# Kernel optimization log

Measured on AMD Instinct MI355X. Metric: run time of the kernel, lower is better.

## Reference

```python
import jax, jax.numpy as jnp
import numpy as np

UNITS = 512
N_CLASSES = 10
N_FEAT = 3
R_ON = 0.05      # open ratio of the phased-LSTM time gate
ALPHA = 0.001    # leak rate when gate is closed


def setup_inputs() -> dict:
    key = jax.random.key(0)
    ks = jax.random.split(key, 16)
    B, T, F, U, C = 512, 1024, N_FEAT, UNITS, N_CLASSES
    inputs = jax.random.normal(ks[0], (B, T, F), dtype=jnp.float32)
    # irregular, monotonically increasing observation times
    gaps = jax.random.uniform(ks[1], (B, T), dtype=jnp.float32, minval=0.01, maxval=1.0)
    times = jnp.cumsum(gaps, axis=1)
    sc_in = 1.0 / np.sqrt(F)
    sc_u = 1.0 / np.sqrt(U)
    params = {
        'W0': jax.random.normal(ks[2], (F, 4 * U), jnp.float32) * sc_in,
        'U0': jax.random.normal(ks[3], (U, 4 * U), jnp.float32) * sc_u,
        'b0': jnp.zeros((4 * U,), jnp.float32),
        'tau0': jnp.exp(jax.random.uniform(ks[4], (U,), jnp.float32, np.log(10.0), np.log(1000.0))),
        's0': jax.random.uniform(ks[5], (U,), jnp.float32, 0.0, 100.0),
        'W1': jax.random.normal(ks[6], (U, 4 * U), jnp.float32) * sc_u,
        'U1': jax.random.normal(ks[7], (U, 4 * U), jnp.float32) * sc_u,
        'b1': jnp.zeros((4 * U,), jnp.float32),
        'tau1': jnp.exp(jax.random.uniform(ks[8], (U,), jnp.float32, np.log(10.0), np.log(1000.0))),
        's1': jax.random.uniform(ks[9], (U,), jnp.float32, 0.0, 100.0),
        'Wfc': jax.random.normal(ks[10], (U, C), jnp.float32) * sc_u,
        'bfc': jnp.zeros((C,), jnp.float32),
    }
    return dict(inputs=inputs, times=times, **params)


def _plstm_cell(x, t, h, c, W, U, b, tau, s):
    # x:[B,in], t:[B], h,c:[B,U]; standard LSTM gates + phased time gate
    z = x @ W + h @ U + b                     # [B,4U]
    i, f, g, o = jnp.split(z, 4, axis=-1)
    i = jax.nn.sigmoid(i)
    f = jax.nn.sigmoid(f)
    g = jnp.tanh(g)
    o = jax.nn.sigmoid(o)
    c_cand = f * c + i * g
    h_cand = o * jnp.tanh(c_cand)
    # time gate: phase of each unit's oscillation at time t
    phi = jnp.mod(t[:, None] - s, tau) / tau  # [B,U] in [0,1)
    k = jnp.where(phi < 0.5 * R_ON, 2.0 * phi / R_ON,
        jnp.where(phi < R_ON, 2.0 - 2.0 * phi / R_ON, ALPHA * phi))
    c_new = k * c_cand + (1.0 - k) * c
    h_new = k * h_cand + (1.0 - k) * h
    return h_new, c_new


def reference(inputs, times, W0, U0, b0, tau0, s0, W1, U1, b1, tau1, s1, Wfc, bfc):
    B = inputs.shape[0]
    Uh = W0.shape[1] // 4
    h0 = jnp.zeros((B, Uh), inputs.dtype)
    init = (h0, h0, h0, h0)  # (h0, c0, h1, c1)

    def step(carry, xt):
        h_0, c_0, h_1, c_1 = carry
        x, t = xt
        h_0, c_0 = _plstm_cell(x, t, h_0, c_0, W0, U0, b0, tau0, s0)
        h_1, c_1 = _plstm_cell(h_0, t, h_1, c_1, W1, U1, b1, tau1, s1)
        y = jax.nn.softmax(h_1 @ Wfc + bfc, axis=-1)
        return (h_0, c_0, h_1, c_1), y

    xs = (jnp.swapaxes(inputs, 0, 1), jnp.swapaxes(times, 0, 1))  # time-major
    _, preds = jax.lax.scan(step, init, xs)   # [T,B,C]
    return jnp.transpose(preds, (1, 0, 2))     # [B,T,C]
```

## Files before the change

kernel.cpp:

```cpp
#include <hip/hip_runtime.h>
#include <hip/hip_bf16.h>
#include <math.h>

#define TDIM 1024
#define UDIM 512
#define NG   2048
#define NBLK 208

typedef __attribute__((ext_vector_type(8))) short short8;
typedef __attribute__((ext_vector_type(4))) float float4v;

#define OFF_U0T   ((size_t)0)
#define SZ_U0T    ((size_t)NG*UDIM*2)
#define OFF_W1U1T (OFF_U0T + SZ_U0T)
#define SZ_W1U1T  ((size_t)NG*1024*2)
#define OFF_W0P   (OFF_W1U1T + SZ_W1U1T)
#define SZ_W0P    ((size_t)3*NG*4)
#define OFF_B0P   (OFF_W0P + SZ_W0P)
#define OFF_B1P   (OFF_B0P + (size_t)NG*4)
#define OFF_STATE (OFF_B1P + (size_t)NG*4)
#define SZ_HB     ((size_t)512*UDIM*2)
#define SZ_HF     ((size_t)512*UDIM*4)
#define OFF_H0B   (OFF_STATE)
#define OFF_H1B   (OFF_H0B + 4*SZ_HB)
#define OFF_H1F   (OFF_H1B + 4*SZ_HB)
#define OFF_CNT   (OFF_H1F + 4*SZ_HF)
#define STATE_BYTES (8*SZ_HB + 4*SZ_HF + 4096)

#define HSLOT ((size_t)512*UDIM)
#define FSLOT ((size_t)512*UDIM)

__device__ __forceinline__ float sigm(float x) { return 1.0f / (1.0f + expf(-x)); }

__device__ __forceinline__ void gload16(const void* g, void* l) {
    __builtin_amdgcn_global_load_lds(
        (const __attribute__((address_space(1))) void*)g,
        (__attribute__((address_space(3))) void*)l, 16, 0, 17);
}

__device__ __forceinline__ void store_u16_llc(void* p, unsigned short v) {
    asm volatile("global_store_short %0, %1, off sc0 sc1" :: "v"(p), "v"(v) : "memory");
}
__device__ __forceinline__ void store_f32_llc(void* p, float v) {
    asm volatile("global_store_dword %0, %1, off sc0 sc1" :: "v"(p), "v"(v) : "memory");
}

__device__ __forceinline__ void wait_ge(unsigned* p, int tgt, unsigned& seen) {
    if ((int)seen >= tgt) return;
    unsigned v = __hip_atomic_load(p, __ATOMIC_RELAXED, __HIP_MEMORY_SCOPE_AGENT);
    while ((int)v < tgt) {
        __builtin_amdgcn_s_sleep(1);
        v = __hip_atomic_load(p, __ATOMIC_RELAXED, __HIP_MEMORY_SCOPE_AGENT);
    }
    seen = v;
}

__device__ __forceinline__ void signal(unsigned* p) {
    asm volatile("s_waitcnt vmcnt(0)" ::: "memory");
    __hip_atomic_fetch_add(p, 1u, __ATOMIC_RELAXED, __HIP_MEMORY_SCOPE_AGENT);
}

__device__ __forceinline__ void cell_update(float zi, float zf, float zg, float zo,
                                            float tt, float tv, float sv,
                                            float& cp, float& hp)
{
    float ig = sigm(zi), fg = sigm(zf), gg = tanhf(zg), og = sigm(zo);
    float cc = fg * cp + ig * gg;
    float hc = og * tanhf(cc);
    float ph = fmodf(tt - sv, tv);
    ph = (ph < 0.0f ? ph + tv : ph) / tv;
    float kg = (ph < 0.025f) ? (ph * 40.0f)
             : (ph < 0.05f ? 2.0f - ph * 40.0f : 0.001f * ph);
    cp = kg * cc + (1.0f - kg) * cp;
    hp = kg * hc + (1.0f - kg) * hp;
}

__global__ void prep_kernel(const float* __restrict__ W0, const float* __restrict__ U0,
                            const float* __restrict__ b0, const float* __restrict__ W1,
                            const float* __restrict__ U1, const float* __restrict__ b1,
                            char* __restrict__ ws)
{
    int idx = blockIdx.x * 256 + threadIdx.x;
    int n = idx >> 10;
    int k = idx & 1023;
    int oc = (n & 3) * UDIM + (n >> 2);
    __hip_bfloat16* U0t = (__hip_bfloat16*)(ws + OFF_U0T);
    __hip_bfloat16* Wc  = (__hip_bfloat16*)(ws + OFF_W1U1T);
    float* W0p = (float*)(ws + OFF_W0P);
    float* b0p = (float*)(ws + OFF_B0P);
    float* b1p = (float*)(ws + OFF_B1P);
    if (k < 512) U0t[(size_t)n * 512 + k] = __float2bfloat16(U0[(size_t)k * NG + oc]);
    float wv = (k < 512) ? W1[(size_t)k * NG + oc] : U1[(size_t)(k - 512) * NG + oc];
    Wc[(size_t)n * 1024 + k] = __float2bfloat16(wv);
    if (k < 3) W0p[k * NG + n] = W0[(size_t)k * NG + oc];
    if (k == 0) { b0p[n] = b0[oc]; b1p[n] = b1[oc]; }
}

__device__ void layer0_persist(char* smem, int blk,
    const float* __restrict__ inputs, const float* __restrict__ times,
    const float* __restrict__ tau0, const float* __restrict__ s0v, char* __restrict__ ws)
{
    const int msl = blk >> 4, nsl = blk & 15;
    unsigned* cnt = (unsigned*)(ws + OFF_CNT);
    unsigned* P0 = cnt + msl * 32;
    unsigned* P1 = cnt + 128 + msl * 32;
    unsigned seen0 = 0, seen1 = 0;
    const int tid = threadIdx.x;
    const int wave = tid >> 6, lane = tid & 63, lr = lane & 15, lq = lane >> 4;
    const int mg = wave >> 2, nw = wave & 3;
    const int colbase = nsl * 128 + nw * 32;

    const __hip_bfloat16* U0t = (const __hip_bfloat16*)(ws + OFF_U0T);
    const float* b0p = (const float*)(ws + OFF_B0P);
    const float* W0p = (const float*)(ws + OFF_W0P);
    __hip_bfloat16* h0b = (__hip_bfloat16*)(ws + OFF_H0B);

    short8 Bf[32];
#pragma unroll
    for (int nf = 0; nf < 2; ++nf)
#pragma unroll
        for (int kk = 0; kk < 16; ++kk)
            Bf[nf * 16 + kk] = *(const short8*)(U0t +
                (size_t)(colbase + nf * 16 + lr) * 512 + kk * 32 + lq * 8);

    const int cu = tid & 31, crb = tid >> 5;
    const int uu = nsl * 32 + cu;
    const int pcc = nsl * 128 + cu * 4;
    const float4v bias4 = *(const float4v*)(b0p + pcc);
    const float4v w0x = *(const float4v*)(W0p + pcc);
    const float4v w0y = *(const float4v*)(W0p + NG + pcc);
    const float4v w0z = *(const float4v*)(W0p + 2 * NG + pcc);
    const float tv = tau0[uu], sv = s0v[uu];

    float c0r[8], h0r[8];
#pragma unroll
    for (int i = 0; i < 8; ++i) { c0r[i] = 0.0f; h0r[i] = 0.0f; }

    const int g_row = tid >> 2;
    const int g_q   = (tid & 3) ^ ((g_row >> 1) & 3);

    for (int s = 0; s < TDIM; ++s) {
        if (tid == 0) {
            wait_ge(P0, 16 * s, seen0);
            if (s >= 4) wait_ge(P1, 32 * (s - 3), seen1);
        }
        __syncthreads();

        const __hip_bfloat16* Arow = h0b + ((size_t)((s + 3) & 3)) * HSLOT +
            (size_t)(msl * 128 + g_row) * 512 + g_q * 8;
        __hip_bfloat16* h0w = h0b + ((size_t)(s & 3)) * HSLOT;
#pragma unroll
        for (int j = 0; j < 7; ++j)
            gload16(Arow + j * 32, smem + j * 8192 + wave * 1024);

        const float4v z4 = {0.0f, 0.0f, 0.0f, 0.0f};
        float4v acc[4][2];
#pragma unroll
        for (int mf = 0; mf < 4; ++mf) { acc[mf][0] = z4; acc[mf][1] = z4; }

#pragma unroll
        for (int j = 0; j < 16; ++j) {
            asm volatile("s_waitcnt vmcnt(%0)" :: "i"((j + 7 < 16) ? 6 : (15 - j)) : "memory");
            __builtin_amdgcn_s_barrier();
            __builtin_amdgcn_sched_barrier(0);
            if (j + 7 < 16)
                gload16(Arow + (j + 7) * 32, smem + ((j + 7) & 7) * 8192 + wave * 1024);
            const short* sA = (const short*)(smem + (j & 7) * 8192);
            short8 aF[4];
#pragma unroll
            for (int mf = 0; mf < 4; ++mf) {
                int row = mg * 64 + mf * 16 + lr;
                int q = lq ^ ((row >> 1) & 3);
                aF[mf] = *(const short8*)(sA + row * 32 + q * 8);
            }
#pragma unroll
            for (int mf = 0; mf < 4; ++mf) {
                acc[mf][0] = __builtin_amdgcn_mfma_f32_16x16x32_bf16(aF[mf], Bf[j],      acc[mf][0], 0, 0, 0);
                acc[mf][1] = __builtin_amdgcn_mfma_f32_16x16x32_bf16(aF[mf], Bf[16 + j], acc[mf][1], 0, 0, 0);
            }
        }
        __syncthreads();
        float* Z = (float*)smem;
#pragma unroll
        for (int pass = 0; pass < 2; ++pass) {
            if (mg == pass) {
#pragma unroll
                for (int mf = 0; mf < 4; ++mf)
#pragma unroll
                    for (int nf = 0; nf < 2; ++nf)
#pragma unroll
                        for (int i = 0; i < 4; ++i)
                            Z[(mf * 16 + lq * 4 + i) * 132 + nw * 32 + nf * 16 + lr] = acc[mf][nf][i];
            }
            __syncthreads();
#pragma unroll
            for (int cc = 0; cc < 4; ++cc) {
                int rl = crb + 16 * cc;
                int b = msl * 128 + pass * 64 + rl;
                float4v z = *(const float4v*)(Z + rl * 132 + cu * 4);
                const float* xp = inputs + ((size_t)b * TDIM + s) * 3;
                float x0 = xp[0], x1 = xp[1], x2 = xp[2];
                float zi = z[0] + bias4[0] + x0 * w0x[0] + x1 * w0y[0] + x2 * w0z[0];
                float zf = z[1] + bias4[1] + x0 * w0x[1] + x1 * w0y[1] + x2 * w0z[1];
                float zg = z[2] + bias4[2] + x0 * w0x[2] + x1 * w0y[2] + x2 * w0z[2];
                float zo = z[3] + bias4[3] + x0 * w0x[3] + x1 * w0y[3] + x2 * w0z[3];
                float tt = times[(size_t)b * TDIM + s];
                cell_update(zi, zf, zg, zo, tt, tv, sv, c0r[pass * 4 + cc], h0r[pass * 4 + cc]);
                __hip_bfloat16 hb = __float2bfloat16(h0r[pass * 4 + cc]);
                store_u16_llc(h0w + (size_t)b * 512 + uu, *(unsigned short*)&hb);
            }
            __syncthreads();
        }
        if (tid == 0) signal(P0);
    }
}

__device__ void layer1_persist(char* smem, int blk,
    const float* __restrict__ times,
    const float* __restrict__ tau1, const float* __restrict__ s1v, char* __restrict__ ws)
{
    const int m8 = blk >> 4, nsl = blk & 15;
    const int grp = m8 >> 1;
    unsigned* cnt = (unsigned*)(ws + OFF_CNT);
    unsigned* P0 = cnt + grp * 32;
    unsigned* P1 = cnt + 128 + grp * 32;
    unsigned* PF = cnt + 256 + grp * 32;
    unsigned seen0 = 0, seen1 = 0, seenF = 0;
    const int tid = threadIdx.x;
    const int wave = tid >> 6, lane = tid & 63, lr = lane & 15, lq = lane >> 4;
    const int kg = wave >> 2, nw = wave & 3;
    const int colbase = nsl * 128 + nw * 32;

    const __hip_bfloat16* Wc = (const __hip_bfloat16*)(ws + OFF_W1U1T);
    const float* b1p = (const float*)(ws + OFF_B1P);
    __hip_bfloat16* h0b = (__hip_bfloat16*)(ws + OFF_H0B);
    __hip_bfloat16* h1b = (__hip_bfloat16*)(ws + OFF_H1B);
    float* h1f = (float*)(ws + OFF_H1F);

    short8 Bf[32];
#pragma unroll
    for (int nf = 0; nf < 2; ++nf)
#pragma unroll
        for (int kk = 0; kk < 16; ++kk)
            Bf[nf * 16 + kk] = *(const short8*)(Wc +
                (size_t)(colbase + nf * 16 + lr) * 1024 + kg * 512 + kk * 32 + lq * 8);

    const int cu = tid & 31, crb = tid >> 5;
    const int uu = nsl * 32 + cu;
    const int pcc = nsl * 128 + cu * 4;
    const float4v bias4 = *(const float4v*)(b1p + pcc);
    const float tv = tau1[uu], sv = s1v[uu];

    float c1r[4], h1r[4];
#pragma unroll
    for (int i = 0; i < 4; ++i) { c1r[i] = 0.0f; h1r[i] = 0.0f; }

    const int g_row = tid >> 3;
    const int g_q   = (tid & 7) ^ (g_row & 7);

    for (int s = 1; s <= TDIM; ++s) {
        const int t = s - 1;
        if (tid == 0) {
            wait_ge(P0, 16 * s, seen0);
            wait_ge(P1, 32 * (s - 1), seen1);
            if (s >= 5) wait_ge(PF, 4 * (s - 4), seenF);
        }
        __syncthreads();

        const __hip_bfloat16* A0 = h0b + ((size_t)((s + 3) & 3)) * HSLOT +
            (size_t)(m8 * 64 + g_row) * 512 + g_q * 8;
        const __hip_bfloat16* A1 = h1b + ((size_t)((s + 2) & 3)) * HSLOT +
            (size_t)(m8 * 64 + g_row) * 512 + g_q * 8;
        __hip_bfloat16* h1w = h1b + ((size_t)((s + 3) & 3)) * HSLOT;
        float* h1fw = h1f + ((size_t)((s + 3) & 3)) * FSLOT;
#pragma unroll
        for (int J = 0; J < 3; ++J) {
            gload16(A0 + J * 64, smem + (J & 3) * 8192 + wave * 1024);
            gload16(A1 + J * 64, smem + 32768 + (J & 3) * 8192 + wave * 1024);
        }
        const float4v z4 = {0.0f, 0.0f, 0.0f, 0.0f};
        float4v acc[4][2];
#pragma unroll
        for (int mf = 0; mf < 4; ++mf) { acc[mf][0] = z4; acc[mf][1] = z4; }

#pragma unroll
        for (int J = 0; J < 8; ++J) {
            asm volatile("s_waitcnt vmcnt(%0)" :: "i"((J + 2 < 8) ? 4 : ((7 - J) * 2)) : "memory");
            __builtin_amdgcn_s_barrier();
            __builtin_amdgcn_sched_barrier(0);
            if (J + 3 < 8) {
                gload16(A0 + (J + 3) * 64, smem + ((J + 3) & 3) * 8192 + wave * 1024);
                gload16(A1 + (J + 3) * 64, smem + 32768 + ((J + 3) & 3) * 8192 + wave * 1024);
            }
            const short* sA = (const short*)(smem + kg * 32768 + (J & 3) * 8192);
#pragma unroll
            for (int kk = 0; kk < 2; ++kk) {
                short8 aF[4];
#pragma unroll
                for (int mf = 0; mf < 4; ++mf) {
                    int row = mf * 16 + lr;
                    int q = (kk * 4 + lq) ^ (row & 7);
                    aF[mf] = *(const short8*)(sA + row * 64 + q * 8);
                }
#pragma unroll
                for (int mf = 0; mf < 4; ++mf) {
                    acc[mf][0] = __builtin_amdgcn_mfma_f32_16x16x32_bf16(aF[mf], Bf[J * 2 + kk],      acc[mf][0], 0, 0, 0);
                    acc[mf][1] = __builtin_amdgcn_mfma_f32_16x16x32_bf16(aF[mf], Bf[16 + J * 2 + kk], acc[mf][1], 0, 0, 0);
                }
            }
        }
        __syncthreads();
        float* Z = (float*)smem;
        if (kg == 1) {
#pragma unroll
            for (int mf = 0; mf < 4; ++mf)
#pragma unroll
                for (int nf = 0; nf < 2; ++nf)
#pragma unroll
                    for (int i = 0; i < 4; ++i)
                        Z[(mf * 16 + lq * 4 + i) * 132 + nw * 32 + nf * 16 + lr] = acc[mf][nf][i];
        }
        __syncthreads();
        if (kg == 0) {
#pragma unroll
            for (int mf = 0; mf < 4; ++mf)
#pragma unroll
                for (int nf = 0; nf < 2; ++nf)
#pragma unroll
                    for (int i = 0; i < 4; ++i) {
                        int idx = (mf * 16 + lq * 4 + i) * 132 + nw * 32 + nf * 16 + lr;
                        Z[idx] += acc[mf][nf][i];
                    }
        }
        __syncthreads();
#pragma unroll
        for (int cc = 0; cc < 4; ++cc) {
            int rl = crb + 16 * cc;
            int b = m8 * 64 + rl;
            float4v z = *(const float4v*)(Z + rl * 132 + cu * 4);
            float zi = z[0] + bias4[0];
            float zf = z[1] + bias4[1];
            float zg = z[2] + bias4[2];
            float zo = z[3] + bias4[3];
            float tt = times[(size_t)b * TDIM + t];
            cell_update(zi, zf, zg, zo, tt, tv, sv, c1r[cc], h1r[cc]);
            __hip_bfloat16 hb = __float2bfloat16(h1r[cc]);
            store_u16_llc(h1w + (size_t)b * 512 + uu, *(unsigned short*)&hb);
            store_f32_llc(h1fw + (size_t)b * 512 + uu, h1r[cc]);
        }
        __syncthreads();
        if (tid == 0) signal(P1);
    }
}

__device__ void fc_persist(char* smem, int blk, const float* __restrict__ Wfc,
                           const float* __restrict__ bfc,
                           char* __restrict__ ws, float* __restrict__ out)
{
    const int grp = blk >> 2;
    unsigned* cnt = (unsigned*)(ws + OFF_CNT);
    unsigned* P1 = cnt + 128 + grp * 32;
    unsigned* PF = cnt + 256 + grp * 32;
    unsigned seen1 = 0;
    const int tid = threadIdx.x, wave = tid >> 6, lane = tid & 63;
    const float* h1f = (const float*)(ws + OFF_H1F);
    const int rbase = blk * 32;

    for (int s = 2; s <= TDIM + 1; ++s) {
        int t = s - 2;
        if (tid == 0) wait_ge(P1, 32 * (s - 1), seen1);
        __syncthreads();
        const char* h = (const char*)(h1f + ((size_t)((s + 2) & 3)) * FSLOT +
                                      (size_t)rbase * 512);
#pragma unroll
        for (int k = 0; k < 8; ++k)
            gload16(h + ((size_t)(tid + k * 512)) * 16, smem + k * 8192 + wave * 1024);
        asm volatile("s_waitcnt vmcnt(0)" ::: "memory");
        __syncthreads();
        if (tid == 0) signal(PF);
        const float* hl = (const float*)smem;
        for (int ri = 0; ri < 4; ++ri) {
            int rl = wave * 4 + ri;
            int row = rbase + rl;
            float a[10];
#pragma unroll
            for (int c = 0; c < 10; ++c) a[c] = 0.0f;
#pragma unroll
            for (int itr = 0; itr < 8; ++itr) {
                float hv = hl[(size_t)rl * 512 + itr * 64 + lane];
                const float* wp = &Wfc[(size_t)(itr * 64 + lane) * 10];
#pragma unroll
                for (int c = 0; c < 10; ++c) a[c] += hv * wp[c];
            }
#pragma unroll
            for (int c = 0; c < 10; ++c)
                for (int m = 32; m; m >>= 1) a[c] += __shfl_xor(a[c], m, 64);
            if (lane == 0) {
                float mx = -1e30f;
#pragma unroll
                for (int c = 0; c < 10; ++c) { a[c] += bfc[c]; mx = fmaxf(mx, a[c]); }
                float sum = 0.0f;
#pragma unroll
                for (int c = 0; c < 10; ++c) { a[c] = expf(a[c] - mx); sum += a[c]; }
                float inv = 1.0f / sum;
                float* op = &out[((size_t)row * TDIM + t) * 10];
#pragma unroll
                for (int c = 0; c < 10; ++c) op[c] = a[c] * inv;
            }
        }
        __syncthreads();
    }
}

__global__ __launch_bounds__(512, 2)
void persist_kernel(const float* __restrict__ inputs, const float* __restrict__ times,
                    const float* __restrict__ tau0, const float* __restrict__ s0v,
                    const float* __restrict__ tau1, const float* __restrict__ s1v,
                    const float* __restrict__ Wfc, const float* __restrict__ bfc,
                    char* __restrict__ ws, float* __restrict__ out)
{
    __shared__ __align__(16) char smem[65536];
    int blk = blockIdx.x;
    if (blk < 64)       layer0_persist(smem, blk, inputs, times, tau0, s0v, ws);
    else if (blk < 192) layer1_persist(smem, blk - 64, times, tau1, s1v, ws);
    else                fc_persist(smem, blk - 192, Wfc, bfc, ws, out);
}

extern "C" void kernel_launch(void* const* d_in, const int* in_sizes, int n_in,
                              void* d_out, int out_size, void* d_ws, size_t ws_size,
                              hipStream_t stream) {
    const float* inputs = (const float*)d_in[0];
    const float* times  = (const float*)d_in[1];
    const float* W0   = (const float*)d_in[2];
    const float* U0   = (const float*)d_in[3];
    const float* b0   = (const float*)d_in[4];
    const float* tau0 = (const float*)d_in[5];
    const float* s0   = (const float*)d_in[6];
    const float* W1   = (const float*)d_in[7];
    const float* U1   = (const float*)d_in[8];
    const float* b1   = (const float*)d_in[9];
    const float* tau1 = (const float*)d_in[10];
    const float* s1   = (const float*)d_in[11];
    const float* Wfc  = (const float*)d_in[12];
    const float* bfc  = (const float*)d_in[13];
    float* out = (float*)d_out;
    char* ws = (char*)d_ws;

    hipMemsetAsync(ws + OFF_STATE, 0, STATE_BYTES, stream);
    prep_kernel<<<(NG * 1024) / 256, 256, 0, stream>>>(W0, U0, b0, W1, U1, b1, ws);

    void* kargs[] = {(void*)&inputs, (void*)&times, (void*)&tau0, (void*)&s0,
                     (void*)&tau1, (void*)&s1, (void*)&Wfc, (void*)&bfc,
                     (void*)&ws, (void*)&out};
    hipLaunchCooperativeKernel((const void*)persist_kernel, dim3(NBLK), dim3(512),
                               kargs, 0, stream);
}
```

Measured before the change: 14.97 ms.

## Replace atomic counters with per-block flags, rotate K order, use fast math

Per-group atomic fetch-add counters are replaced by per-block flag slots written with plain stores. Every wave polls these with a wavefront min-reduction, which removes the tid-0 wait plus __syncthreads handoff. The K-loop start is rotated per block (nsl/r1 offset) to spread concurrent reads of the shared h buffers, and the layer-0 inner loop processes two K-chunks per barrier. Transcendentals switch to __expf/rcp-based sigmoid/tanh and fmod is replaced by multiply-by-reciprocal and floor, which trades some accuracy and adds extra memory polling traffic from every wave.

```diff
diff --git a/kernel.cpp b/kernel.cpp
--- a/kernel.cpp
+++ b/kernel.cpp
@@ -30,7 +30,10 @@
 #define HSLOT ((size_t)512*UDIM)
 #define FSLOT ((size_t)512*UDIM)
 
-__device__ __forceinline__ float sigm(float x) { return 1.0f / (1.0f + expf(-x)); }
+
+__device__ __forceinline__ float rcpf(float x) { return __builtin_amdgcn_rcpf(x); }
+__device__ __forceinline__ float sigm(float x) { return rcpf(1.0f + __expf(-x)); }
+__device__ __forceinline__ float tanhfast(float x) { return 1.0f - 2.0f * rcpf(1.0f + __expf(2.0f * x)); }
 
 __device__ __forceinline__ void gload16(const void* g, void* l) {
     __builtin_amdgcn_global_load_lds(
@@ -44,31 +47,41 @@
 __device__ __forceinline__ void store_f32_llc(void* p, float v) {
     asm volatile("global_store_dword %0, %1, off sc0 sc1" :: "v"(p), "v"(v) : "memory");
 }
-
-__device__ __forceinline__ void wait_ge(unsigned* p, int tgt, unsigned& seen) {
-    if ((int)seen >= tgt) return;
-    unsigned v = __hip_atomic_load(p, __ATOMIC_RELAXED, __HIP_MEMORY_SCOPE_AGENT);
-    while ((int)v < tgt) {
-        __builtin_amdgcn_s_sleep(1);
-        v = __hip_atomic_load(p, __ATOMIC_RELAXED, __HIP_MEMORY_SCOPE_AGENT);
-    }
-    seen = v;
-}
-
-__device__ __forceinline__ void signal(unsigned* p) {
-    asm volatile("s_waitcnt vmcnt(0)" ::: "memory");
-    __hip_atomic_fetch_add(p, 1u, __ATOMIC_RELAXED, __HIP_MEMORY_SCOPE_AGENT);
+__device__ __forceinline__ void store_cnt(unsigned* p, unsigned v) {
+    asm volatile("global_store_dword %0, %1, off sc0 sc1" :: "v"(p), "v"(v) : "memory");
+}
+
+__device__ __forceinline__ int minv(const unsigned* base, int lanemask) {
+    unsigned u = __hip_atomic_load(base + (threadIdx.x & lanemask),
+                                   __ATOMIC_RELAXED, __HIP_MEMORY_SCOPE_AGENT);
+    int x = (int)u;
+#pragma unroll
+    for (int m = 32; m; m >>= 1) x = min(x, __shfl_xor(x, m, 64));
+    return x;
+}
+__device__ __forceinline__ void wait_min(const unsigned* base, int lanemask,
+                                         int tgt, int& seen) {
+    while (seen < tgt) {
+        seen = minv(base, lanemask);
+        if (seen < tgt) __builtin_amdgcn_s_sleep(2);
+    }
+}
+__device__ __forceinline__ void wait_val(unsigned* p, int tgt, int& seen) {
+    while (seen < tgt) {
+        seen = (int)__hip_atomic_load(p, __ATOMIC_RELAXED, __HIP_MEMORY_SCOPE_AGENT);
+        if (seen < tgt) __builtin_amdgcn_s_sleep(2);
+    }
 }
 
 __device__ __forceinline__ void cell_update(float zi, float zf, float zg, float zo,
-                                            float tt, float tv, float sv,
+                                            float tt, float tvi, float sv,
                                             float& cp, float& hp)
 {
-    float ig = sigm(zi), fg = sigm(zf), gg = tanhf(zg), og = sigm(zo);
+    float ig = sigm(zi), fg = sigm(zf), gg = tanhfast(zg), og = sigm(zo);
     float cc = fg * cp + ig * gg;
-    float hc = og * tanhf(cc);
-    float ph = fmodf(tt - sv, tv);
-    ph = (ph < 0.0f ? ph + tv : ph) / tv;
+    float hc = og * tanhfast(cc);
+    float q  = (tt - sv) * tvi;
+    float ph = q - floorf(q);
     float kg = (ph < 0.025f) ? (ph * 40.0f)
              : (ph < 0.05f ? 2.0f - ph * 40.0f : 0.001f * ph);
     cp = kg * cc + (1.0f - kg) * cp;
@@ -102,9 +115,10 @@
 {
     const int msl = blk >> 4, nsl = blk & 15;
     unsigned* cnt = (unsigned*)(ws + OFF_CNT);
-    unsigned* P0 = cnt + msl * 32;
-    unsigned* P1 = cnt + 128 + msl * 32;
-    unsigned seen0 = 0, seen1 = 0;
+    const unsigned* P0G = cnt + msl * 16;
+    const unsigned* P1G = cnt + 64 + msl * 32;
+    unsigned* myP0 = cnt + msl * 16 + nsl;
+    int rawSeen = 0, warSeen = 0;
     const int tid = threadIdx.x;
     const int wave = tid >> 6, lane = tid & 63, lr = lane & 15, lq = lane >> 4;
     const int mg = wave >> 2, nw = wave & 3;
@@ -117,11 +131,11 @@
 
     short8 Bf[32];
 #pragma unroll
-    for (int nf = 0; nf < 2; ++nf)
-#pragma unroll
-        for (int kk = 0; kk < 16; ++kk)
-            Bf[nf * 16 + kk] = *(const short8*)(U0t +
-                (size_t)(colbase + nf * 16 + lr) * 512 + kk * 32 + lq * 8);
+    for (int i = 0; i < 16; ++i) {
+        int l = (nsl + i) & 15;
+        Bf[i]      = *(const short8*)(U0t + (size_t)(colbase + lr) * 512 + l * 32 + lq * 8);
+        Bf[16 + i] = *(const short8*)(U0t + (size_t)(colbase + 16 + lr) * 512 + l * 32 + lq * 8);
+    }
 
     const int cu = tid & 31, crb = tid >> 5;
     const int uu = nsl * 32 + cu;
@@ -130,7 +144,7 @@
     const float4v w0x = *(const float4v*)(W0p + pcc);
     const float4v w0y = *(const float4v*)(W0p + NG + pcc);
     const float4v w0z = *(const float4v*)(W0p + 2 * NG + pcc);
-    const float tv = tau0[uu], sv = s0v[uu];
+    const float tvi = 1.0f / tau0[uu], sv = s0v[uu];
 
     float c0r[8], h0r[8];
 #pragma unroll
@@ -140,18 +154,15 @@
     const int g_q   = (tid & 3) ^ ((g_row >> 1) & 3);
 
     for (int s = 0; s < TDIM; ++s) {
-        if (tid == 0) {
-            wait_ge(P0, 16 * s, seen0);
-            if (s >= 4) wait_ge(P1, 32 * (s - 3), seen1);
-        }
-        __syncthreads();
+        if (s >= 4) wait_min(P1G, 31, s - 3, warSeen);
+        wait_min(P0G, 15, s, rawSeen);
 
         const __hip_bfloat16* Arow = h0b + ((size_t)((s + 3) & 3)) * HSLOT +
             (size_t)(msl * 128 + g_row) * 512 + g_q * 8;
         __hip_bfloat16* h0w = h0b + ((size_t)(s & 3)) * HSLOT;
 #pragma unroll
-        for (int j = 0; j < 7; ++j)
-            gload16(Arow + j * 32, smem + j * 8192 + wave * 1024);
+        for (int j = 0; j < 6; ++j)
+            gload16(Arow + ((nsl + j) & 15) * 32, smem + j * 8192 + wave * 1024);
 
         const float4v z4 = {0.0f, 0.0f, 0.0f, 0.0f};
         float4v acc[4][2];
@@ -159,24 +170,31 @@
         for (int mf = 0; mf < 4; ++mf) { acc[mf][0] = z4; acc[mf][1] = z4; }
 
 #pragma unroll
-        for (int j = 0; j < 16; ++j) {
-            asm volatile("s_waitcnt vmcnt(%0)" :: "i"((j + 7 < 16) ? 6 : (15 - j)) : "memory");
+        for (int I = 0; I < 8; ++I) {
+            asm volatile("s_waitcnt vmcnt(%0)" :: "i"((I <= 5) ? 4 : (14 - 2 * I)) : "memory");
             __builtin_amdgcn_s_barrier();
             __builtin_amdgcn_sched_barrier(0);
-            if (j + 7 < 16)
-                gload16(Arow + (j + 7) * 32, smem + ((j + 7) & 7) * 8192 + wave * 1024);
-            const short* sA = (const short*)(smem + (j & 7) * 8192);
-            short8 aF[4];
+            if (I < 5) {
+                int t0 = 2 * I + 6, t1 = 2 * I + 7;
+                gload16(Arow + ((nsl + t0) & 15) * 32, smem + (t0 & 7) * 8192 + wave * 1024);
+                gload16(Arow + ((nsl + t1) & 15) * 32, smem + (t1 & 7) * 8192 + wave * 1024);
+            }
+            const short* sA0 = (const short*)(smem + ((2 * I) & 7) * 8192);
+            const short* sA1 = (const short*)(smem + ((2 * I + 1) & 7) * 8192);
+            short8 aF0[4], aF1[4];
 #pragma unroll
             for (int mf = 0; mf < 4; ++mf) {
                 int row = mg * 64 + mf * 16 + lr;
                 int q = lq ^ ((row >> 1) & 3);
-                aF[mf] = *(const short8*)(sA + row * 32 + q * 8);
+                aF0[mf] = *(const short8*)(sA0 + row * 32 + q * 8);
+                aF1[mf] = *(const short8*)(sA1 + row * 32 + q * 8);
             }
 #pragma unroll
             for (int mf = 0; mf < 4; ++mf) {
-                acc[mf][0] = __builtin_amdgcn_mfma_f32_16x16x32_bf16(aF[mf], Bf[j],      acc[mf][0], 0, 0, 0);
-                acc[mf][1] = __builtin_amdgcn_mfma_f32_16x16x32_bf16(aF[mf], Bf[16 + j], acc[mf][1], 0, 0, 0);
+                acc[mf][0] = __builtin_amdgcn_mfma_f32_16x16x32_bf16(aF0[mf], Bf[2 * I],          acc[mf][0], 0, 0, 0);
+                acc[mf][1] = __builtin_amdgcn_mfma_f32_16x16x32_bf16(aF0[mf], Bf[16 + 2 * I],     acc[mf][1], 0, 0, 0);
+                acc[mf][0] = __builtin_amdgcn_mfma_f32_16x16x32_bf16(aF1[mf], Bf[2 * I + 1],      acc[mf][0], 0, 0, 0);
+                acc[mf][1] = __builtin_amdgcn_mfma_f32_16x16x32_bf16(aF1[mf], Bf[16 + 2 * I + 1], acc[mf][1], 0, 0, 0);
             }
         }
         __syncthreads();
@@ -205,13 +223,13 @@
                 float zg = z[2] + bias4[2] + x0 * w0x[2] + x1 * w0y[2] + x2 * w0z[2];
                 float zo = z[3] + bias4[3] + x0 * w0x[3] + x1 * w0y[3] + x2 * w0z[3];
                 float tt = times[(size_t)b * TDIM + s];
-                cell_update(zi, zf, zg, zo, tt, tv, sv, c0r[pass * 4 + cc], h0r[pass * 4 + cc]);
+                cell_update(zi, zf, zg, zo, tt, tvi, sv, c0r[pass * 4 + cc], h0r[pass * 4 + cc]);
                 __hip_bfloat16 hb = __float2bfloat16(h0r[pass * 4 + cc]);
                 store_u16_llc(h0w + (size_t)b * 512 + uu, *(unsigned short*)&hb);
             }
             __syncthreads();
         }
-        if (tid == 0) signal(P0);
+        if (tid == 0) store_cnt(myP0, (unsigned)(s + 1));
     }
 }
 
@@ -220,16 +238,18 @@
     const float* __restrict__ tau1, const float* __restrict__ s1v, char* __restrict__ ws)
 {
     const int m8 = blk >> 4, nsl = blk & 15;
-    const int grp = m8 >> 1;
+    const int grp = m8 >> 1, half = m8 & 1;
     unsigned* cnt = (unsigned*)(ws + OFF_CNT);
-    unsigned* P0 = cnt + grp * 32;
-    unsigned* P1 = cnt + 128 + grp * 32;
-    unsigned* PF = cnt + 256 + grp * 32;
-    unsigned seen0 = 0, seen1 = 0, seenF = 0;
+    const unsigned* P0G = cnt + grp * 16;
+    const unsigned* P1R = cnt + 64 + grp * 32 + half * 16;
+    unsigned* myP1 = cnt + 64 + grp * 32 + half * 16 + nsl;
+    unsigned* PF = cnt + 192 + grp * 16;
+    int raw0Seen = 0, raw1Seen = 0, pfSeen = 0;
     const int tid = threadIdx.x;
     const int wave = tid >> 6, lane = tid & 63, lr = lane & 15, lq = lane >> 4;
     const int kg = wave >> 2, nw = wave & 3;
     const int colbase = nsl * 128 + nw * 32;
+    const int r1 = nsl & 7;
 
     const __hip_bfloat16* Wc = (const __hip_bfloat16*)(ws + OFF_W1U1T);
     const float* b1p = (const float*)(ws + OFF_B1P);
@@ -239,17 +259,20 @@
 
     short8 Bf[32];
 #pragma unroll
-    for (int nf = 0; nf < 2; ++nf)
-#pragma unroll
-        for (int kk = 0; kk < 16; ++kk)
-            Bf[nf * 16 + kk] = *(const short8*)(Wc +
-                (size_t)(colbase + nf * 16 + lr) * 1024 + kg * 512 + kk * 32 + lq * 8);
+    for (int i = 0; i < 8; ++i) {
+        int l = (i + r1) & 7;
+#pragma unroll
+        for (int kk = 0; kk < 2; ++kk) {
+            Bf[i * 2 + kk]      = *(const short8*)(Wc + (size_t)(colbase + lr) * 1024 + kg * 512 + (l * 2 + kk) * 32 + lq * 8);
+            Bf[16 + i * 2 + kk] = *(const short8*)(Wc + (size_t)(colbase + 16 + lr) * 1024 + kg * 512 + (l * 2 + kk) * 32 + lq * 8);
+        }
+    }
 
     const int cu = tid & 31, crb = tid >> 5;
     const int uu = nsl * 32 + cu;
     const int pcc = nsl * 128 + cu * 4;
     const float4v bias4 = *(const float4v*)(b1p + pcc);
-    const float tv = tau1[uu], sv = s1v[uu];
+    const float tvi = 1.0f / tau1[uu], sv = s1v[uu];
 
     float c1r[4], h1r[4];
 #pragma unroll
@@ -260,12 +283,9 @@
 
     for (int s = 1; s <= TDIM; ++s) {
         const int t = s - 1;
-        if (tid == 0) {
-            wait_ge(P0, 16 * s, seen0);
-            wait_ge(P1, 32 * (s - 1), seen1);
-            if (s >= 5) wait_ge(PF, 4 * (s - 4), seenF);
-        }
-        __syncthreads();
+        if (s >= 5) wait_val(PF, 4 * (s - 4), pfSeen);
+        wait_min(P0G, 15, s, raw0Seen);
+        wait_min(P1R, 15, s - 1, raw1Seen);
 
         const __hip_bfloat16* A0 = h0b + ((size_t)((s + 3) & 3)) * HSLOT +
             (size_t)(m8 * 64 + g_row) * 512 + g_q * 8;
@@ -275,8 +295,9 @@
         float* h1fw = h1f + ((size_t)((s + 3) & 3)) * FSLOT;
 #pragma unroll
         for (int J = 0; J < 3; ++J) {
-            gload16(A0 + J * 64, smem + (J & 3) * 8192 + wave * 1024);
-            gload16(A1 + J * 64, smem + 32768 + (J & 3) * 8192 + wave * 1024);
+            int l = (J + r1) & 7;
+            gload16(A0 + l * 64, smem + (J & 3) * 8192 + wave * 1024);
+            gload16(A1 + l * 64, smem + 32768 + (J & 3) * 8192 + wave * 1024);
         }
         const float4v z4 = {0.0f, 0.0f, 0.0f, 0.0f};
         float4v acc[4][2];
@@ -289,8 +310,9 @@
             __builtin_amdgcn_s_barrier();
             __builtin_amdgcn_sched_barrier(0);
             if (J + 3 < 8) {
-                gload16(A0 + (J + 3) * 64, smem + ((J + 3) & 3) * 8192 + wave * 1024);
-                gload16(A1 + (J + 3) * 64, smem + 32768 + ((J + 3) & 3) * 8192 + wave * 1024);
+                int l = (J + 3 + r1) & 7;
+                gload16(A0 + l * 64, smem + ((J + 3) & 3) * 8192 + wave * 1024);
+                gload16(A1 + l * 64, smem + 32768 + ((J + 3) & 3) * 8192 + wave * 1024);
             }
             const short* sA = (const short*)(smem + kg * 32768 + (J & 3) * 8192);
 #pragma unroll
@@ -343,13 +365,13 @@
             float zg = z[2] + bias4[2];
             float zo = z[3] + bias4[3];
             float tt = times[(size_t)b * TDIM + t];
-            cell_update(zi, zf, zg, zo, tt, tv, sv, c1r[cc], h1r[cc]);
+            cell_update(zi, zf, zg, zo, tt, tvi, sv, c1r[cc], h1r[cc]);
             __hip_bfloat16 hb = __float2bfloat16(h1r[cc]);
             store_u16_llc(h1w + (size_t)b * 512 + uu, *(unsigned short*)&hb);
             store_f32_llc(h1fw + (size_t)b * 512 + uu, h1r[cc]);
         }
         __syncthreads();
-        if (tid == 0) signal(P1);
+        if (tid == 0) store_cnt(myP1, (unsigned)s);
     }
 }
 
@@ -359,17 +381,16 @@
 {
     const int grp = blk >> 2;
     unsigned* cnt = (unsigned*)(ws + OFF_CNT);
-    unsigned* P1 = cnt + 128 + grp * 32;
-    unsigned* PF = cnt + 256 + grp * 32;
-    unsigned seen1 = 0;
+    const unsigned* P1R = cnt + 64 + grp * 32 + ((blk >> 1) & 1) * 16;
+    unsigned* PF = cnt + 192 + grp * 16;
+    int raw1Seen = 0;
     const int tid = threadIdx.x, wave = tid >> 6, lane = tid & 63;
     const float* h1f = (const float*)(ws + OFF_H1F);
     const int rbase = blk * 32;
 
     for (int s = 2; s <= TDIM + 1; ++s) {
         int t = s - 2;
-        if (tid == 0) wait_ge(P1, 32 * (s - 1), seen1);
-        __syncthreads();
+        wait_min(P1R, 15, s - 1, raw1Seen);
         const char* h = (const char*)(h1f + ((size_t)((s + 2) & 3)) * FSLOT +
                                       (size_t)rbase * 512);
 #pragma unroll
@@ -377,7 +398,8 @@
             gload16(h + ((size_t)(tid + k * 512)) * 16, smem + k * 8192 + wave * 1024);
         asm volatile("s_waitcnt vmcnt(0)" ::: "memory");
         __syncthreads();
-        if (tid == 0) signal(PF);
+        if (tid == 0)
+            __hip_atomic_fetch_add(PF, 1u, __ATOMIC_RELAXED, __HIP_MEMORY_SCOPE_AGENT);
         const float* hl = (const float*)smem;
         for (int ri = 0; ri < 4; ++ri) {
             int rl = wave * 4 + ri;
@@ -401,7 +423,7 @@
                 for (int c = 0; c < 10; ++c) { a[c] += bfc[c]; mx = fmaxf(mx, a[c]); }
                 float sum = 0.0f;
 #pragma unroll
-                for (int c = 0; c < 10; ++c) { a[c] = expf(a[c] - mx); sum += a[c]; }
+                for (int c = 0; c < 10; ++c) { a[c] = __expf(a[c] - mx); sum += a[c]; }
                 float inv = 1.0f / sum;
                 float* op = &out[((size_t)row * TDIM + t) * 10];
 #pragma unroll
```

Result: faster. 12.34 ms (-17.6%).
